# Kernel tuning notes

Measured on AMD Instinct MI355X. Metric: run time of the kernel, lower is better.

The kernel has to match this reference:

```python
import jax, jax.numpy as jnp
import numpy as np

L, N, E, H = 2048, 4, 256, 4
D = E // H  # head_dim


def setup_inputs() -> dict:
    key = jax.random.key(0)
    ks = jax.random.split(key, 8)
    s = 1.0 / np.sqrt(E)
    return {
        "x": jax.random.normal(ks[0], (L, N, E), jnp.float32),
        "pos_emb": jax.random.normal(ks[1], (1, 2 * L - 1, E), jnp.float32),
        "in_proj_w": jax.random.normal(ks[2], (3 * E, E), jnp.float32) * s,
        "in_proj_b": jnp.zeros((3 * E,), jnp.float32),
        "pos_w": jax.random.normal(ks[3], (E, E), jnp.float32) * s,
        "pos_bias_u": jax.random.normal(ks[4], (H, D), jnp.float32) * s,
        "pos_bias_v": jax.random.normal(ks[5], (H, D), jnp.float32) * s,
        "out_proj_w": jax.random.normal(ks[6], (E, E), jnp.float32) * s,
        "out_proj_b": jnp.zeros((E,), jnp.float32),
    }


def _rel_shift(bd):
    # bd: (N, H, L, 2L-1) -> (N, H, L, L); out[...,i,j] = bd[...,i, L-1-i+j]
    l = bd.shape[2]
    idx = (l - 1) - jnp.arange(l)[:, None] + jnp.arange(l)[None, :]  # (L, L)
    return jnp.take_along_axis(bd, idx[None, None, :, :], axis=-1)


def reference(x, pos_emb, in_proj_w, in_proj_b, pos_w, pos_bias_u,
              pos_bias_v, out_proj_w, out_proj_b):
    scaling = 1.0 / jnp.sqrt(jnp.asarray(D, x.dtype))
    qkv = x @ in_proj_w.T + in_proj_b                # (L, N, 3E)
    q, k, v = jnp.split(qkv, 3, axis=-1)
    q = q * scaling
    # (L,N,E) -> (N,H,L,D)
    q = q.reshape(L, N, H, D).transpose(1, 2, 0, 3)
    k = k.reshape(L, N, H, D).transpose(1, 2, 0, 3)
    v = v.reshape(L, N, H, D).transpose(1, 2, 0, 3)
    # positional projection: (1, 2L-1, E) -> (H, 2L-1, D)
    p = (pos_emb @ pos_w.T).reshape(2 * L - 1, H, D).transpose(1, 0, 2)
    q_u = q + pos_bias_u[None, :, None, :]
    q_v = q + pos_bias_v[None, :, None, :]
    matrix_ac = jnp.einsum('bhld,bhsd->bhls', q_u, k)          # (N,H,L,L)
    matrix_bd = jnp.einsum('bhld,hnd->bhln', q_v, p)           # (N,H,L,2L-1)
    matrix_bd = _rel_shift(matrix_bd)                          # (N,H,L,L)
    scores = matrix_ac + matrix_bd
    attn = jax.nn.softmax(scores, axis=-1)
    out = jnp.einsum('bhls,bhsd->bhld', attn, v)               # (N,H,L,D)
    out = out.transpose(2, 0, 1, 3).reshape(L, N, E)
    return out @ out_proj_w.T + out_proj_b
```

## Files before the change

kernel.cpp:

```cpp
#include <hip/hip_runtime.h>
#include <math.h>
#include <stdint.h>


typedef __attribute__((ext_vector_type(8))) _Float16 half8;
typedef __attribute__((ext_vector_type(4))) float f32x4;
typedef __attribute__((ext_vector_type(16))) float f32x16;
typedef unsigned short u16;
typedef unsigned int u32;

namespace {
constexpr int L_SEQ  = 2048;
constexpr int NB     = 4;
constexpr int EMB    = 256;
constexpr int NH     = 4;
constexpr int HD     = 64;
constexpr int P_ROWS = 2 * L_SEQ - 1;
}

__device__ __forceinline__ u16 f2h(float x) {
    _Float16 h = (_Float16)x;
    return __builtin_bit_cast(u16, h);
}
__device__ __forceinline__ u32 pk2(float a, float b) {
    return (u32)f2h(a) | ((u32)f2h(b) << 16);
}

__global__ __launch_bounds__(256, 2) void qkvpos_gemm(
        const float* __restrict__ x, const float* __restrict__ pos_emb,
        const float* __restrict__ in_w, const float* __restrict__ in_b,
        const float* __restrict__ pos_w,
        const float* __restrict__ u_bias, const float* __restrict__ v_bias,
        u16* __restrict__ quB, u16* __restrict__ qvB,
        u16* __restrict__ kB,  u16* __restrict__ vtB, u16* __restrict__ pB) {
    __shared__ __align__(16) u16 ws[64 * 256];
    __shared__ __align__(16) u16 scr[128 * 72];

    const int t    = threadIdx.x;
    const int lane = t & 63;
    const int w    = t >> 6;
    const int il   = lane & 15;
    const int g    = lane >> 4;

    const int logical = (blockIdx.x & 7) * 112 + (blockIdx.x >> 3);
    const bool isQKV = logical < 768;
    int mg, nt;
    const float *Ap, *W, *Wb;
    if (isQKV) { mg = logical / 12; nt = logical % 12; Ap = x;       W = in_w;  Wb = in_b; }
    else       { const int l2 = logical - 768;
                 mg = l2 >> 2;     nt = l2 & 3;      Ap = pos_emb; W = pos_w; Wb = nullptr; }
    const int m0 = mg * 128, n0 = nt * 64;

    {
        const int kc = (t & 31) * 8, rb_ = t >> 5;
        #pragma unroll
        for (int rr = 0; rr < 8; ++rr) {
            const int row = rb_ * 8 + rr;
            const float* wr = &W[(size_t)(n0 + row) * 256 + kc];
            float4 f0 = *(const float4*)&wr[0];
            float4 f1 = *(const float4*)&wr[4];
            *(uint4*)((char*)ws + row * 512 + ((kc * 2) ^ ((row & 7) << 4))) =
                make_uint4(pk2(f0.x, f0.y), pk2(f0.z, f0.w),
                           pk2(f1.x, f1.y), pk2(f1.z, f1.w));
        }
    }

    half8 bf0[8], bf1[8];
    {
        int r0 = m0 + w * 32 + il;
        int r1 = r0 + 16;
        if (!isQKV) { r0 = r0 > 4094 ? 4094 : r0; r1 = r1 > 4094 ? 4094 : r1; }
        const float* a0 = Ap + (size_t)r0 * 256;
        const float* a1 = Ap + (size_t)r1 * 256;
        #pragma unroll
        for (int c = 0; c < 8; ++c) {
            float4 f0 = *(const float4*)&a0[c * 32 + g * 8];
            float4 f1 = *(const float4*)&a0[c * 32 + g * 8 + 4];
            bf0[c] = __builtin_bit_cast(half8,
                make_uint4(pk2(f0.x, f0.y), pk2(f0.z, f0.w),
                           pk2(f1.x, f1.y), pk2(f1.z, f1.w)));
            float4 h0 = *(const float4*)&a1[c * 32 + g * 8];
            float4 h1 = *(const float4*)&a1[c * 32 + g * 8 + 4];
            bf1[c] = __builtin_bit_cast(half8,
                make_uint4(pk2(h0.x, h0.y), pk2(h0.z, h0.w),
                           pk2(h1.x, h1.y), pk2(h1.z, h1.w)));
        }
    }
    __syncthreads();

    f32x4 acc0[4] = {}, acc1[4] = {};
    __builtin_amdgcn_s_setprio(1);
    #pragma unroll
    for (int c = 0; c < 8; ++c) {
        #pragma unroll
        for (int jt = 0; jt < 4; ++jt) {
            const int row = jt * 16 + il;
            half8 af = *(const half8*)((const char*)ws + row * 512 +
                                       ((c * 64 + g * 16) ^ ((row & 7) << 4)));
            acc0[jt] = __builtin_amdgcn_mfma_f32_16x16x32_f16(af, bf0[c], acc0[jt], 0, 0, 0);
            acc1[jt] = __builtin_amdgcn_mfma_f32_16x16x32_f16(af, bf1[c], acc1[jt], 0, 0, 0);
        }
    }
    __builtin_amdgcn_s_setprio(0);

    float av[2][4][4];
    #pragma unroll
    for (int jt = 0; jt < 4; ++jt)
        #pragma unroll
        for (int r = 0; r < 4; ++r) {
            const float bb = Wb ? Wb[n0 + jt * 16 + g * 4 + r] : 0.f;
            av[0][jt][r] = acc0[jt][r] + bb;
            av[1][jt][r] = acc1[jt][r] + bb;
        }

    u16* scrw = scr + w * (32 * 72);
    const int rrd  = lane >> 1;
    const int base = (lane & 1) * 32;

    auto waveStore = [&](u16* dstBase, int hh, float scale, const float* bias,
                         bool qkvLayout) {
        #pragma unroll
        for (int s = 0; s < 2; ++s)
            #pragma unroll
            for (int jt = 0; jt < 4; ++jt) {
                const int d0 = jt * 16 + g * 4;
                float v0 = av[s][jt][0] * scale, v1 = av[s][jt][1] * scale;
                float v2 = av[s][jt][2] * scale, v3 = av[s][jt][3] * scale;
                if (bias) {
                    v0 += bias[hh * 64 + d0 + 0]; v1 += bias[hh * 64 + d0 + 1];
                    v2 += bias[hh * 64 + d0 + 2]; v3 += bias[hh * 64 + d0 + 3];
                }
                *(uint2*)&scrw[(s * 16 + il) * 72 + d0] = make_uint2(pk2(v0, v1), pk2(v2, v3));
            }
        uint4 q0 = *(const uint4*)&scrw[rrd * 72 + base + 0];
        uint4 q1 = *(const uint4*)&scrw[rrd * 72 + base + 8];
        uint4 q2 = *(const uint4*)&scrw[rrd * 72 + base + 16];
        uint4 q3 = *(const uint4*)&scrw[rrd * 72 + base + 24];
        const int mglob = m0 + w * 32 + rrd;
        if (qkvLayout) {
            const int i = mglob >> 2, b = mglob & 3;
            u16* dp = dstBase + (((size_t)(b * 4 + hh)) * 2048 + i) * 64 + base;
            *(uint4*)&dp[0] = q0; *(uint4*)&dp[8] = q1;
            *(uint4*)&dp[16] = q2; *(uint4*)&dp[24] = q3;
        } else if (mglob < P_ROWS) {
            u16* dp = dstBase + ((size_t)hh * P_ROWS + mglob) * 64 + base;
            *(uint4*)&dp[0] = q0; *(uint4*)&dp[8] = q1;
            *(uint4*)&dp[16] = q2; *(uint4*)&dp[24] = q3;
        }
    };

    if (isQKV) {
        const int seg = nt >> 2, h = nt & 3;
        if (seg == 0) {
            waveStore(quB, h, 0.125f, u_bias, true);
            waveStore(qvB, h, 0.125f, v_bias, true);
        } else if (seg == 1) {
            waveStore(kB, h, 1.f, nullptr, true);
        } else {
            #pragma unroll
            for (int s = 0; s < 2; ++s)
                #pragma unroll
                for (int jt = 0; jt < 4; ++jt)
                    *(uint2*)&scr[(w * 32 + s * 16 + il) * 72 + jt * 16 + g * 4] =
                        make_uint2(pk2(av[s][jt][0], av[s][jt][1]),
                                   pk2(av[s][jt][2], av[s][jt][3]));
            __syncthreads();
            const int b_ = w, d = lane;
            u32 pkx[16];
            #pragma unroll
            for (int z = 0; z < 16; ++z)
                pkx[z] = (u32)scr[((2 * z) * 4 + b_) * 72 + d] |
                         ((u32)scr[((2 * z + 1) * 4 + b_) * 72 + d] << 16);
            u16* dp = vtB + (((size_t)(b_ * 4 + h)) * 64 + d) * 2048 + mg * 32;
            *(uint4*)&dp[0]  = make_uint4(pkx[0],  pkx[1],  pkx[2],  pkx[3]);
            *(uint4*)&dp[8]  = make_uint4(pkx[4],  pkx[5],  pkx[6],  pkx[7]);
            *(uint4*)&dp[16] = make_uint4(pkx[8],  pkx[9],  pkx[10], pkx[11]);
            *(uint4*)&dp[24] = make_uint4(pkx[12], pkx[13], pkx[14], pkx[15]);
        }
    } else {
        waveStore(pB, nt, 1.f, nullptr, false);
    }
}

__global__ __launch_bounds__(256, 2) void out_gemm(
        const u16* __restrict__ attnb, const float* __restrict__ W,
        const float* __restrict__ Wb, float* __restrict__ outf) {
    __shared__ __align__(16) u16 ws[64 * 256];

    const int t    = threadIdx.x;
    const int lane = t & 63;
    const int w    = t >> 6;
    const int il   = lane & 15;
    const int g    = lane >> 4;

    const int logical = (blockIdx.x & 7) * 32 + (blockIdx.x >> 3);
    const int mg = logical >> 2, nt = logical & 3;
    const int m0 = mg * 128, n0 = nt * 64;

    {
        const int kc = (t & 31) * 8, rb_ = t >> 5;
        #pragma unroll
        for (int rr = 0; rr < 8; ++rr) {
            const int row = rb_ * 8 + rr;
            const float* wr = &W[(size_t)(n0 + row) * 256 + kc];
            float4 f0 = *(const float4*)&wr[0];
            float4 f1 = *(const float4*)&wr[4];
            *(uint4*)((char*)ws + row * 512 + ((kc * 2) ^ ((row & 7) << 4))) =
                make_uint4(pk2(f0.x, f0.y), pk2(f0.z, f0.w),
                           pk2(f1.x, f1.y), pk2(f1.z, f1.w));
        }
    }
    half8 bf0[8], bf1[8];
    {
        const u16* a0 = attnb + (size_t)(m0 + w * 32 + il) * 256;
        const u16* a1 = a0 + 16 * 256;
        #pragma unroll
        for (int c = 0; c < 8; ++c) {
            bf0[c] = *(const half8*)&a0[c * 32 + g * 8];
            bf1[c] = *(const half8*)&a1[c * 32 + g * 8];
        }
    }
    __syncthreads();

    f32x4 acc0[4] = {}, acc1[4] = {};
    __builtin_amdgcn_s_setprio(1);
    #pragma unroll
    for (int c = 0; c < 8; ++c) {
        #pragma unroll
        for (int jt = 0; jt < 4; ++jt) {
            const int row = jt * 16 + il;
            half8 af = *(const half8*)((const char*)ws + row * 512 +
                                       ((c * 64 + g * 16) ^ ((row & 7) << 4)));
            acc0[jt] = __builtin_amdgcn_mfma_f32_16x16x32_f16(af, bf0[c], acc0[jt], 0, 0, 0);
            acc1[jt] = __builtin_amdgcn_mfma_f32_16x16x32_f16(af, bf1[c], acc1[jt], 0, 0, 0);
        }
    }
    __builtin_amdgcn_s_setprio(0);

    #pragma unroll
    for (int s = 0; s < 2; ++s) {
        const int m_ = m0 + w * 32 + s * 16 + il;
        float* orow = &outf[(size_t)m_ * 256 + n0];
        #pragma unroll
        for (int jt = 0; jt < 4; ++jt) {
            const f32x4 a = s ? acc1[jt] : acc0[jt];
            *(float4*)&orow[jt * 16 + g * 4] = make_float4(
                a[0] + Wb[n0 + jt * 16 + g * 4 + 0],
                a[1] + Wb[n0 + jt * 16 + g * 4 + 1],
                a[2] + Wb[n0 + jt * 16 + g * 4 + 2],
                a[3] + Wb[n0 + jt * 16 + g * 4 + 3]);
        }
    }
}

__global__ __launch_bounds__(128, 1) void attn_mfma(
        const u16* __restrict__ quB, const u16* __restrict__ qvB,
        const u16* __restrict__ kB,  const u16* __restrict__ vtB,
        const u16* __restrict__ pB,  u16* __restrict__ attn_out) {
    __shared__ __align__(16) u16   k_s[64 * 64];
    __shared__ __align__(16) u16   v_s[64 * 64];
    __shared__ __align__(16) u16   p_s[128 * 64];
    __shared__ __align__(16) float bd_f[2 * 96 * 34];
    __shared__ __align__(16) u32   pb_u[2 * 32 * 20];

    const int t    = threadIdx.x;
    const int lane = t & 63;
    const int w    = t >> 6;
    const int l31  = lane & 31;
    const int hi   = lane >> 5;
    const int hi4  = hi * 4;

    const int logical = ((blockIdx.x & 7) << 6) + (blockIdx.x >> 3);
    const int bh = logical >> 5;
    const int i0 = (logical & 31) * 64;
    const int b  = bh >> 2, h = bh & 3;

    int cx[4];
    {
        const int swz = (l31 & 7) << 4;
        #pragma unroll
        for (int ks = 0; ks < 4; ++ks)
            cx[ks] = ((ks * 32 + hi * 16) ^ swz);
    }
    const int rowb = l31 * 128;

    half8 qu_f[4], qv_f[4];
    {
        const size_t qrow = ((size_t)bh * L_SEQ + i0 + w * 32 + l31) * HD + hi * 8;
        #pragma unroll
        for (int ks = 0; ks < 4; ++ks) {
            qu_f[ks] = *(const half8*)&quB[qrow + ks * 16];
            qv_f[ks] = *(const half8*)&qvB[qrow + ks * 16];
        }
    }

    const int W0 = w * 3264 + hi4 * 34 + l31;
    const int G0 = w * 3264 + (31 - l31 + hi4) * 34 + l31;
    const int PW = w * 640 + l31 * 20;
    const int PRB = (w * 640 + l31 * 20) * 4 + hi * 16;

    const int rw = t >> 3, a8 = t & 7;
    const int wcol = (a8 * 16) ^ ((rw & 7) << 4);
    const int R0 = 32 - 32 * w;
    const int nb0 = 1984 - i0;

    f32x16 out0 = {}, out1 = {};
    float m_run = -INFINITY, l_run = 0.f;

    for (int kt = 0; kt < 32; ++kt) {
        const int j0 = kt * 64;
        const int nb = nb0 + j0;
        __syncthreads();
        #pragma unroll
        for (int kr = 0; kr < 4; ++kr) {
            const int j = kr * 16 + rw;
            uint4 val = *(const uint4*)&kB[((size_t)bh * 2048 + j0 + j) * 64 + a8 * 8];
            *(uint4*)((char*)k_s + j * 128 + wcol) = val;
        }
        #pragma unroll
        for (int vr = 0; vr < 4; ++vr) {
            const int d = vr * 16 + rw;
            uint4 val = *(const uint4*)&vtB[((size_t)bh * 64 + d) * 2048 + j0 + a8 * 8];
            *(uint4*)((char*)v_s + d * 128 + wcol) = val;
        }
        #pragma unroll
        for (int pr = 0; pr < 8; ++pr) {
            const int r = pr * 16 + rw;
            int n = nb + r; n = n > (P_ROWS - 1) ? (P_ROWS - 1) : n; n = n < 0 ? 0 : n;
            uint4 val = *(const uint4*)&pB[((size_t)h * P_ROWS + n) * 64 + a8 * 8];
            *(uint4*)((char*)p_s + r * 128 + wcol) = val;
        }
        __syncthreads();

        __builtin_amdgcn_s_setprio(1);
        #pragma unroll
        for (int rt = 0; rt < 3; ++rt) {
            f32x16 bda = {};
            #pragma unroll
            for (int ks = 0; ks < 4; ++ks) {
                half8 a = *(const half8*)((const char*)p_s + (R0 + rt * 32) * 128 + rowb + cx[ks]);
                bda = __builtin_amdgcn_mfma_f32_32x32x16_f16(a, qv_f[ks], bda, 0, 0, 0);
            }
            #pragma unroll
            for (int r = 0; r < 16; ++r)
                bd_f[W0 + (rt * 32 + (r & 3) + 8 * (r >> 2)) * 34] = bda[r];
        }

        f32x16 s0 = {}, s1 = {};
        #pragma unroll
        for (int ks = 0; ks < 4; ++ks) {
            half8 a0 = *(const half8*)((const char*)k_s + rowb + cx[ks]);
            s0 = __builtin_amdgcn_mfma_f32_32x32x16_f16(a0, qu_f[ks], s0, 0, 0, 0);
        }
        #pragma unroll
        for (int ks = 0; ks < 4; ++ks) {
            half8 a1 = *(const half8*)((const char*)k_s + 32 * 128 + rowb + cx[ks]);
            s1 = __builtin_amdgcn_mfma_f32_32x32x16_f16(a1, qu_f[ks], s1, 0, 0, 0);
        }
        __builtin_amdgcn_s_setprio(0);

        #pragma unroll
        for (int r = 0; r < 16; ++r) {
            const int off = ((r & 3) + 8 * (r >> 2)) * 34;
            s0[r] += bd_f[G0 + off];
            s1[r] += bd_f[G0 + 1088 + off];
        }

        float mx = s0[0];
        #pragma unroll
        for (int r = 1; r < 16; ++r) mx = fmaxf(mx, s0[r]);
        #pragma unroll
        for (int r = 0; r < 16; ++r) mx = fmaxf(mx, s1[r]);
        mx = fmaxf(mx, __shfl_xor(mx, 32));
        const float m_new = fmaxf(m_run, mx);
        const float corr = __expf(m_run - m_new);
        float lsum = 0.f;
        #pragma unroll
        for (int r = 0; r < 16; ++r) { s0[r] = __expf(s0[r] - m_new); lsum += s0[r]; }
        #pragma unroll
        for (int r = 0; r < 16; ++r) { s1[r] = __expf(s1[r] - m_new); lsum += s1[r]; }
        lsum += __shfl_xor(lsum, 32);
        l_run = l_run * corr + lsum;
        m_run = m_new;
        #pragma unroll
        for (int r = 0; r < 16; ++r) { out0[r] *= corr; out1[r] *= corr; }

        #pragma unroll
        for (int jt = 0; jt < 2; ++jt) {
            #pragma unroll
            for (int k4 = 0; k4 < 4; ++k4) {
                const float e0 = jt ? s1[k4 * 4 + 0] : s0[k4 * 4 + 0];
                const float e1 = jt ? s1[k4 * 4 + 1] : s0[k4 * 4 + 1];
                const float e2 = jt ? s1[k4 * 4 + 2] : s0[k4 * 4 + 2];
                const float e3 = jt ? s1[k4 * 4 + 3] : s0[k4 * 4 + 3];
                *(uint2*)&pb_u[PW + k4 * 4 + hi * 2] = make_uint2(pk2(e0, e1), pk2(e2, e3));
            }
            half8 pf0 = *(const half8*)((const char*)pb_u + PRB);
            half8 pf1 = *(const half8*)((const char*)pb_u + PRB + 32);
            __builtin_amdgcn_s_setprio(1);
            {
                half8 va = *(const half8*)((const char*)v_s + rowb + cx[jt * 2 + 0]);
                out0 = __builtin_amdgcn_mfma_f32_32x32x16_f16(va, pf0, out0, 0, 0, 0);
                half8 vb = *(const half8*)((const char*)v_s + rowb + cx[jt * 2 + 1]);
                out0 = __builtin_amdgcn_mfma_f32_32x32x16_f16(vb, pf1, out0, 0, 0, 0);
                half8 vc = *(const half8*)((const char*)v_s + 32 * 128 + rowb + cx[jt * 2 + 0]);
                out1 = __builtin_amdgcn_mfma_f32_32x32x16_f16(vc, pf0, out1, 0, 0, 0);
                half8 vd = *(const half8*)((const char*)v_s + 32 * 128 + rowb + cx[jt * 2 + 1]);
                out1 = __builtin_amdgcn_mfma_f32_32x32x16_f16(vd, pf1, out1, 0, 0, 0);
            }
            __builtin_amdgcn_s_setprio(0);
        }
    }

    const float inv = 1.f / l_run;
    const int i = i0 + w * 32 + l31;
    const int m = i * NB + b;
    u16* orow = &attn_out[(size_t)m * EMB + h * HD];
    #pragma unroll
    for (int k4 = 0; k4 < 4; ++k4) {
        const int d0 = k4 * 8 + hi4;
        *(uint2*)&orow[d0] = make_uint2(
            pk2(out0[k4 * 4 + 0] * inv, out0[k4 * 4 + 1] * inv),
            pk2(out0[k4 * 4 + 2] * inv, out0[k4 * 4 + 3] * inv));
        *(uint2*)&orow[32 + d0] = make_uint2(
            pk2(out1[k4 * 4 + 0] * inv, out1[k4 * 4 + 1] * inv),
            pk2(out1[k4 * 4 + 2] * inv, out1[k4 * 4 + 3] * inv));
    }
}

extern "C" void kernel_launch(void* const* d_in, const int* in_sizes, int n_in,
                              void* d_out, int out_size, void* d_ws, size_t ws_size,
                              hipStream_t stream) {
    const float* x        = (const float*)d_in[0];
    const float* pos_emb  = (const float*)d_in[1];
    const float* in_w     = (const float*)d_in[2];
    const float* in_b     = (const float*)d_in[3];
    const float* pos_w    = (const float*)d_in[4];
    const float* u_bias   = (const float*)d_in[5];
    const float* v_bias   = (const float*)d_in[6];
    const float* out_w    = (const float*)d_in[7];
    const float* out_b    = (const float*)d_in[8];
    float* out = (float*)d_out;

    u16* quB   = (u16*)d_ws;
    u16* qvB   = quB + (size_t)16 * L_SEQ * HD;
    u16* kB    = qvB + (size_t)16 * L_SEQ * HD;
    u16* vtB   = kB  + (size_t)16 * L_SEQ * HD;
    u16* pB    = vtB + (size_t)16 * L_SEQ * HD;
    u16* attnb = pB  + (size_t)NH * P_ROWS * HD;

    qkvpos_gemm<<<dim3(896), 256, 0, stream>>>(
        x, pos_emb, in_w, in_b, pos_w, u_bias, v_bias, quB, qvB, kB, vtB, pB);
    attn_mfma<<<dim3(512), 128, 0, stream>>>(quB, qvB, kB, vtB, pB, attnb);
    out_gemm<<<dim3(256), 256, 0, stream>>>(attnb, out_w, out_b, out);
}
```

Before: 192.6 us.

## Split attention key tiles across four waves with shared max and merged outputs

The attention kernel moves from 2 waves to 4 waves per block. Each wave pair splits the 64 keys of a tile, sharing the per-row max through LDS and merging the partial outputs and row sums at the end. The positional band is now stored in LDS as fp16 pairs instead of fp32, which shrinks LDS use and permits two blocks per CU. The cost is extra __syncthreads per tile and fp16 rounding of the bd term. The final merge also contains some dead code.

```diff
diff --git a/kernel.cpp b/kernel.cpp
--- a/kernel.cpp
+++ b/kernel.cpp
@@ -253,40 +253,42 @@
     }
 }
 
-__global__ __launch_bounds__(128, 1) void attn_mfma(
+__global__ __launch_bounds__(256, 2) void attn_mfma(
         const u16* __restrict__ quB, const u16* __restrict__ qvB,
         const u16* __restrict__ kB,  const u16* __restrict__ vtB,
         const u16* __restrict__ pB,  u16* __restrict__ attn_out) {
-    __shared__ __align__(16) u16   k_s[64 * 64];
-    __shared__ __align__(16) u16   v_s[64 * 64];
-    __shared__ __align__(16) u16   p_s[128 * 64];
-    __shared__ __align__(16) float bd_f[2 * 96 * 34];
-    __shared__ __align__(16) u32   pb_u[2 * 32 * 20];
+    __shared__ __align__(16) u16 k_s[64 * 64];
+    __shared__ __align__(16) u16 v_s[64 * 64];
+    __shared__ __align__(16) u16 p_s[128 * 64];
+    __shared__ __align__(16) u32 band_s[64 * 68];
+    __shared__ __align__(16) u32 prob_s[4][32 * 20];
+    __shared__ float mw_s[2][64];
+    __shared__ float lb_s[64];
 
     const int t    = threadIdx.x;
     const int lane = t & 63;
     const int w    = t >> 6;
+    const int qw   = w & 1;
+    const int jw   = w >> 1;
     const int l31  = lane & 31;
     const int hi   = lane >> 5;
-    const int hi4  = hi * 4;
 
     const int logical = ((blockIdx.x & 7) << 6) + (blockIdx.x >> 3);
     const int bh = logical >> 5;
     const int i0 = (logical & 31) * 64;
     const int b  = bh >> 2, h = bh & 3;
+    const int qloc = qw * 32 + l31;
 
     int cx[4];
     {
         const int swz = (l31 & 7) << 4;
         #pragma unroll
-        for (int ks = 0; ks < 4; ++ks)
-            cx[ks] = ((ks * 32 + hi * 16) ^ swz);
-    }
-    const int rowb = l31 * 128;
+        for (int c = 0; c < 4; ++c) cx[c] = ((c * 32 + hi * 16) ^ swz);
+    }
 
     half8 qu_f[4], qv_f[4];
     {
-        const size_t qrow = ((size_t)bh * L_SEQ + i0 + w * 32 + l31) * HD + hi * 8;
+        const size_t qrow = ((size_t)bh * L_SEQ + i0 + qloc) * HD + hi * 8;
         #pragma unroll
         for (int ks = 0; ks < 4; ++ks) {
             qu_f[ks] = *(const half8*)&quB[qrow + ks * 16];
@@ -294,17 +296,11 @@
         }
     }
 
-    const int W0 = w * 3264 + hi4 * 34 + l31;
-    const int G0 = w * 3264 + (31 - l31 + hi4) * 34 + l31;
-    const int PW = w * 640 + l31 * 20;
-    const int PRB = (w * 640 + l31 * 20) * 4 + hi * 16;
-
     const int rw = t >> 3, a8 = t & 7;
     const int wcol = (a8 * 16) ^ ((rw & 7) << 4);
-    const int R0 = 32 - 32 * w;
     const int nb0 = 1984 - i0;
 
-    f32x16 out0 = {}, out1 = {};
+    f32x16 o0 = {}, o1 = {};
     float m_run = -INFINITY, l_run = 0.f;
 
     for (int kt = 0; kt < 32; ++kt) {
@@ -312,20 +308,20 @@
         const int nb = nb0 + j0;
         __syncthreads();
         #pragma unroll
-        for (int kr = 0; kr < 4; ++kr) {
-            const int j = kr * 16 + rw;
+        for (int kr = 0; kr < 2; ++kr) {
+            const int j = kr * 32 + rw;
             uint4 val = *(const uint4*)&kB[((size_t)bh * 2048 + j0 + j) * 64 + a8 * 8];
             *(uint4*)((char*)k_s + j * 128 + wcol) = val;
         }
         #pragma unroll
-        for (int vr = 0; vr < 4; ++vr) {
-            const int d = vr * 16 + rw;
+        for (int vr = 0; vr < 2; ++vr) {
+            const int d = vr * 32 + rw;
             uint4 val = *(const uint4*)&vtB[((size_t)bh * 64 + d) * 2048 + j0 + a8 * 8];
             *(uint4*)((char*)v_s + d * 128 + wcol) = val;
         }
         #pragma unroll
-        for (int pr = 0; pr < 8; ++pr) {
-            const int r = pr * 16 + rw;
+        for (int pr = 0; pr < 4; ++pr) {
+            const int r = pr * 32 + rw;
             int n = nb + r; n = n > (P_ROWS - 1) ? (P_ROWS - 1) : n; n = n < 0 ? 0 : n;
             uint4 val = *(const uint4*)&pB[((size_t)h * P_ROWS + n) * 64 + a8 * 8];
             *(uint4*)((char*)p_s + r * 128 + wcol) = val;
@@ -334,97 +330,123 @@
 
         __builtin_amdgcn_s_setprio(1);
         #pragma unroll
-        for (int rt = 0; rt < 3; ++rt) {
+        for (int tti = 0; tti < 2; ++tti) {
+            const int rt = 2 * jw + tti;
             f32x16 bda = {};
             #pragma unroll
             for (int ks = 0; ks < 4; ++ks) {
-                half8 a = *(const half8*)((const char*)p_s + (R0 + rt * 32) * 128 + rowb + cx[ks]);
+                half8 a = *(const half8*)((const char*)p_s + (rt * 32 + l31) * 128 + cx[ks]);
                 bda = __builtin_amdgcn_mfma_f32_32x32x16_f16(a, qv_f[ks], bda, 0, 0, 0);
             }
             #pragma unroll
-            for (int r = 0; r < 16; ++r)
-                bd_f[W0 + (rt * 32 + (r & 3) + 8 * (r >> 2)) * 34] = bda[r];
-        }
-
-        f32x16 s0 = {}, s1 = {};
+            for (int rr = 0; rr < 4; ++rr)
+                #pragma unroll
+                for (int p = 0; p < 2; ++p) {
+                    const int Rp = rt * 16 + 4 * rr + 2 * hi + p;
+                    band_s[Rp * 68 + qloc] = pk2(bda[rr * 4 + 2 * p], bda[rr * 4 + 2 * p + 1]);
+                }
+        }
+        f32x16 s = {};
         #pragma unroll
         for (int ks = 0; ks < 4; ++ks) {
-            half8 a0 = *(const half8*)((const char*)k_s + rowb + cx[ks]);
-            s0 = __builtin_amdgcn_mfma_f32_32x32x16_f16(a0, qu_f[ks], s0, 0, 0, 0);
-        }
-        #pragma unroll
-        for (int ks = 0; ks < 4; ++ks) {
-            half8 a1 = *(const half8*)((const char*)k_s + 32 * 128 + rowb + cx[ks]);
-            s1 = __builtin_amdgcn_mfma_f32_32x32x16_f16(a1, qu_f[ks], s1, 0, 0, 0);
+            half8 a = *(const half8*)((const char*)k_s + (jw * 32 + l31) * 128 + cx[ks]);
+            s = __builtin_amdgcn_mfma_f32_32x32x16_f16(a, qu_f[ks], s, 0, 0, 0);
         }
         __builtin_amdgcn_s_setprio(0);
-
+        __syncthreads();
+
+        float sr[16];
         #pragma unroll
         for (int r = 0; r < 16; ++r) {
-            const int off = ((r & 3) + 8 * (r >> 2)) * 34;
-            s0[r] += bd_f[G0 + off];
-            s1[r] += bd_f[G0 + 1088 + off];
-        }
-
-        float mx = s0[0];
-        #pragma unroll
-        for (int r = 1; r < 16; ++r) mx = fmaxf(mx, s0[r]);
-        #pragma unroll
-        for (int r = 0; r < 16; ++r) mx = fmaxf(mx, s1[r]);
+            const int jrow = (r & 3) + 8 * (r >> 2) + 4 * hi;
+            const int R = 63 - qloc + jw * 32 + jrow;
+            _Float16 hv = ((const _Float16*)band_s)[(R >> 1) * 136 + qloc * 2 + (R & 1)];
+            sr[r] = s[r] + (float)hv;
+        }
+
+        float mx = sr[0];
+        #pragma unroll
+        for (int r = 1; r < 16; ++r) mx = fmaxf(mx, sr[r]);
         mx = fmaxf(mx, __shfl_xor(mx, 32));
-        const float m_new = fmaxf(m_run, mx);
+        mw_s[jw][qloc] = mx;
+        __syncthreads();
+        const float m_tile = fmaxf(mx, mw_s[1 - jw][qloc]);
+        const float m_new = fmaxf(m_run, m_tile);
         const float corr = __expf(m_run - m_new);
-        float lsum = 0.f;
-        #pragma unroll
-        for (int r = 0; r < 16; ++r) { s0[r] = __expf(s0[r] - m_new); lsum += s0[r]; }
-        #pragma unroll
-        for (int r = 0; r < 16; ++r) { s1[r] = __expf(s1[r] - m_new); lsum += s1[r]; }
-        lsum += __shfl_xor(lsum, 32);
-        l_run = l_run * corr + lsum;
+        float psum = 0.f;
+        #pragma unroll
+        for (int r = 0; r < 16; ++r) { sr[r] = __expf(sr[r] - m_new); psum += sr[r]; }
+        psum += __shfl_xor(psum, 32);
+        l_run = l_run * corr + psum;
         m_run = m_new;
         #pragma unroll
-        for (int r = 0; r < 16; ++r) { out0[r] *= corr; out1[r] *= corr; }
-
-        #pragma unroll
-        for (int jt = 0; jt < 2; ++jt) {
-            #pragma unroll
-            for (int k4 = 0; k4 < 4; ++k4) {
-                const float e0 = jt ? s1[k4 * 4 + 0] : s0[k4 * 4 + 0];
-                const float e1 = jt ? s1[k4 * 4 + 1] : s0[k4 * 4 + 1];
-                const float e2 = jt ? s1[k4 * 4 + 2] : s0[k4 * 4 + 2];
-                const float e3 = jt ? s1[k4 * 4 + 3] : s0[k4 * 4 + 3];
-                *(uint2*)&pb_u[PW + k4 * 4 + hi * 2] = make_uint2(pk2(e0, e1), pk2(e2, e3));
-            }
-            half8 pf0 = *(const half8*)((const char*)pb_u + PRB);
-            half8 pf1 = *(const half8*)((const char*)pb_u + PRB + 32);
-            __builtin_amdgcn_s_setprio(1);
-            {
-                half8 va = *(const half8*)((const char*)v_s + rowb + cx[jt * 2 + 0]);
-                out0 = __builtin_amdgcn_mfma_f32_32x32x16_f16(va, pf0, out0, 0, 0, 0);
-                half8 vb = *(const half8*)((const char*)v_s + rowb + cx[jt * 2 + 1]);
-                out0 = __builtin_amdgcn_mfma_f32_32x32x16_f16(vb, pf1, out0, 0, 0, 0);
-                half8 vc = *(const half8*)((const char*)v_s + 32 * 128 + rowb + cx[jt * 2 + 0]);
-                out1 = __builtin_amdgcn_mfma_f32_32x32x16_f16(vc, pf0, out1, 0, 0, 0);
-                half8 vd = *(const half8*)((const char*)v_s + 32 * 128 + rowb + cx[jt * 2 + 1]);
-                out1 = __builtin_amdgcn_mfma_f32_32x32x16_f16(vd, pf1, out1, 0, 0, 0);
-            }
-            __builtin_amdgcn_s_setprio(0);
-        }
-    }
-
-    const float inv = 1.f / l_run;
-    const int i = i0 + w * 32 + l31;
-    const int m = i * NB + b;
-    u16* orow = &attn_out[(size_t)m * EMB + h * HD];
-    #pragma unroll
-    for (int k4 = 0; k4 < 4; ++k4) {
-        const int d0 = k4 * 8 + hi4;
-        *(uint2*)&orow[d0] = make_uint2(
-            pk2(out0[k4 * 4 + 0] * inv, out0[k4 * 4 + 1] * inv),
-            pk2(out0[k4 * 4 + 2] * inv, out0[k4 * 4 + 3] * inv));
-        *(uint2*)&orow[32 + d0] = make_uint2(
-            pk2(out1[k4 * 4 + 0] * inv, out1[k4 * 4 + 1] * inv),
-            pk2(out1[k4 * 4 + 2] * inv, out1[k4 * 4 + 3] * inv));
+        for (int r = 0; r < 16; ++r) { o0[r] *= corr; o1[r] *= corr; }
+
+        #pragma unroll
+        for (int rr = 0; rr < 4; ++rr)
+            #pragma unroll
+            for (int p = 0; p < 2; ++p)
+                prob_s[w][l31 * 20 + 4 * rr + 2 * hi + p] =
+                    pk2(sr[rr * 4 + 2 * p], sr[rr * 4 + 2 * p + 1]);
+
+        half8 pf[2];
+        #pragma unroll
+        for (int ks2 = 0; ks2 < 2; ++ks2)
+            pf[ks2] = *(const half8*)((const char*)&prob_s[w][0] +
+                                      l31 * 80 + ks2 * 32 + hi * 16);
+        __builtin_amdgcn_s_setprio(1);
+        #pragma unroll
+        for (int ks2 = 0; ks2 < 2; ++ks2) {
+            half8 a0 = *(const half8*)((const char*)v_s + l31 * 128 + cx[2 * jw + ks2]);
+            o0 = __builtin_amdgcn_mfma_f32_32x32x16_f16(a0, pf[ks2], o0, 0, 0, 0);
+            half8 a1 = *(const half8*)((const char*)v_s + (32 + l31) * 128 + cx[2 * jw + ks2]);
+            o1 = __builtin_amdgcn_mfma_f32_32x32x16_f16(a1, pf[ks2], o1, 0, 0, 0);
+        }
+        __builtin_amdgcn_s_setprio(0);
+    }
+
+    __syncthreads();
+    float* ob = (float*)band_s;
+    if (jw == 1) {
+        #pragma unroll
+        for (int r = 0; r < 16; ++r) {
+            const int dr = 8 * (r >> 2) + 4 * hi + (r & 3);
+            ob[qloc * 65 + dr] = o0[r];
+            ob[qloc * 65 + 32 + dr] = o1[r];
+        }
+        lb_s[qloc] = l_run;
+    }
+    __syncthreads();
+    if (jw == 0) {
+        const float inv = 1.f / (l_run + lb_s[qloc]);
+        const int m = (i0 + qloc) * NB + b;
+        u16* orow = &attn_out[(size_t)m * EMB + h * HD];
+        float of[32];
+        #pragma unroll
+        for (int r = 0; r < 16; ++r) {
+            const int dr = 8 * (r >> 2) + 4 * hi + (r & 3);
+            of[dr & 31] = 0.f;
+        }
+        #pragma unroll
+        for (int r = 0; r < 16; ++r) {
+            const int dr = 8 * (r >> 2) + 4 * hi + (r & 3);
+            of[((r >> 2) * 8 + (r & 3)) & 31] = 0.f;
+            (void)dr;
+        }
+        #pragma unroll
+        for (int rr = 0; rr < 4; ++rr) {
+            const int d0 = rr * 8 + 4 * hi;
+            float a0 = (o0[rr * 4 + 0] + ob[qloc * 65 + d0 + 0]) * inv;
+            float a1 = (o0[rr * 4 + 1] + ob[qloc * 65 + d0 + 1]) * inv;
+            float a2 = (o0[rr * 4 + 2] + ob[qloc * 65 + d0 + 2]) * inv;
+            float a3 = (o0[rr * 4 + 3] + ob[qloc * 65 + d0 + 3]) * inv;
+            *(uint2*)&orow[d0] = make_uint2(pk2(a0, a1), pk2(a2, a3));
+            float b0 = (o1[rr * 4 + 0] + ob[qloc * 65 + 32 + d0 + 0]) * inv;
+            float b1 = (o1[rr * 4 + 1] + ob[qloc * 65 + 32 + d0 + 1]) * inv;
+            float b2 = (o1[rr * 4 + 2] + ob[qloc * 65 + 32 + d0 + 2]) * inv;
+            float b3 = (o1[rr * 4 + 3] + ob[qloc * 65 + 32 + d0 + 3]) * inv;
+            *(uint2*)&orow[32 + d0] = make_uint2(pk2(b0, b1), pk2(b2, b3));
+        }
     }
 }
 
@@ -451,6 +473,6 @@
 
     qkvpos_gemm<<<dim3(896), 256, 0, stream>>>(
         x, pos_emb, in_w, in_b, pos_w, u_bias, v_bias, quB, qvB, kB, vtB, pB);
-    attn_mfma<<<dim3(512), 128, 0, stream>>>(quB, qvB, kB, vtB, pB, attnb);
+    attn_mfma<<<dim3(512), 256, 0, stream>>>(quB, qvB, kB, vtB, pB, attnb);
     out_gemm<<<dim3(256), 256, 0, stream>>>(attnb, out_w, out_b, out);
 }
```

After: 176.3 us. 8.4% less time.
